# Performance work log

Hardware: AMD Instinct MI355X
Metric: run time of the kernel (lower is better)

## Reference

```python
import jax, jax.numpy as jnp
import numpy as np

B, T, D, H = 8, 4096, 512, 512


def setup_inputs() -> dict:
    key = jax.random.key(0)
    k1, k2, k3, k4, k5, k6 = jax.random.split(key, 6)
    lim = 1.0 / np.sqrt(D)
    return {
        "x": jax.random.normal(k1, (B, T, D), dtype=jnp.float32),
        "h_0": jax.random.normal(k2, (B, 1, H), dtype=jnp.float32),
        "W_z": jax.random.uniform(k3, (H, D), jnp.float32, -lim, lim),
        "b_z": jax.random.uniform(k4, (H,), jnp.float32, -lim, lim),
        "W_h": jax.random.uniform(k5, (H, D), jnp.float32, -lim, lim),
        "b_h": jax.random.uniform(k6, (H,), jnp.float32, -lim, lim),
    }


def reference(x, h_0, W_z, b_z, W_h, b_h):
    # z_t = sigmoid(W_z x_t), h~_t = tanh(W_h x_t)
    z = jax.nn.sigmoid(jnp.einsum('btd,hd->bth', x, W_z) + b_z)  # (B,T,H)
    h_tilde = jnp.tanh(jnp.einsum('btd,hd->bth', x, W_h) + b_h)  # (B,T,H)
    a = 1.0 - z            # multiplicative coeffs
    b = z * h_tilde        # additive terms (b[:,0] handled as h0 carry)

    # linear recurrence h_t = a_t * h_{t-1} + b_t, h_0 given
    def scan_fn(h_prev, ab):
        a_t, b_t = ab
        h_t = a_t * h_prev + b_t
        return h_t, h_t

    a_t = jnp.swapaxes(a, 0, 1)  # (T,B,H)
    b_t = jnp.swapaxes(b, 0, 1)  # (T,B,H)
    _, hs = jax.lax.scan(scan_fn, h_0[:, 0, :], (a_t, b_t))
    return jnp.swapaxes(hs, 0, 1)  # (B,T,H)
```

## Files before the change

### kernel.cpp

```cpp
#include <hip/hip_runtime.h>

constexpr int Bn = 8, Tn = 4096, Dn = 512, Hn = 512;
constexpr int Mn = Bn * Tn;
constexpr int BM = 128, BHt = 128, BK = 32;
constexpr int NKT = Dn / BK;
constexpr int CH = 64, NC = Tn / CH;

typedef __attribute__((ext_vector_type(8))) short s8v;
typedef __attribute__((ext_vector_type(4))) float f4v;
typedef __attribute__((ext_vector_type(8))) _Float16 h8v;
typedef unsigned short ushort_t;

__device__ __forceinline__ short f2bf(float f) {
  unsigned u = __float_as_uint(f);
  u = (u + 0x7fffu + ((u >> 16) & 1u)) >> 16;
  return (short)u;
}

__global__ __launch_bounds__(256) void convert_all(
    const float* __restrict__ X, const float* __restrict__ Wz,
    const float* __restrict__ Wh, ushort_t* __restrict__ Xb,
    ushort_t* __restrict__ Wzb, ushort_t* __restrict__ Whb) {
  int bx = blockIdx.x, tid = threadIdx.x;
  const float* src;
  ushort_t* dst;
  int lb;
  if (bx < 4096)      { src = X;  dst = Xb;  lb = bx; }
  else if (bx < 4160) { src = Wz; dst = Wzb; lb = bx - 4096; }
  else                { src = Wh; dst = Whb; lb = bx - 4160; }
  const float* tsrc = src + ((size_t)(lb >> 4) * 128) * Dn + (lb & 15) * BK;
#pragma unroll
  for (int p = 0; p < 2; p++) {
    int idx = tid + p * 256;
    int r = idx >> 2, k8 = idx & 3;
    const float4* sv = reinterpret_cast<const float4*>(tsrc + (size_t)r * Dn + k8 * 8);
    float4 f0 = sv[0], f1 = sv[1];
    s8v v;
    v[0] = f2bf(f0.x); v[1] = f2bf(f0.y); v[2] = f2bf(f0.z); v[3] = f2bf(f0.w);
    v[4] = f2bf(f1.x); v[5] = f2bf(f1.y); v[6] = f2bf(f1.z); v[7] = f2bf(f1.w);
    int c = (r >> 4) * 64 + k8 * 16 + (r & 15);
    *reinterpret_cast<s8v*>(&dst[((size_t)lb * 512 + c) * 8]) = v;
  }
}

__global__ __launch_bounds__(256, 2) void gemm_act(
    const ushort_t* __restrict__ Xb, const ushort_t* __restrict__ Wzb,
    const ushort_t* __restrict__ Whb,
    const float* __restrict__ bzp, const float* __restrict__ bhp,
    h8v* __restrict__ cab) {
  int tid = threadIdx.x, lane = tid & 63, wid = tid >> 6;
  int wr = wid >> 1, wc = wid & 1;
  int bm = blockIdx.x, bhb = blockIdx.y;

  const s8v* xs = reinterpret_cast<const s8v*>(Xb) + (size_t)bm * NKT * 512 + (wr * 4) * 64 + lane;
  const s8v* zs = reinterpret_cast<const s8v*>(Wzb) + (size_t)bhb * NKT * 512 + (wc * 4) * 64 + lane;
  const s8v* hs = reinterpret_cast<const s8v*>(Whb) + (size_t)bhb * NKT * 512 + (wc * 4) * 64 + lane;

  f4v accz[4][4], acch[4][4];
#pragma unroll
  for (int i = 0; i < 4; i++)
#pragma unroll
    for (int j = 0; j < 4; j++) {
      accz[i][j] = (f4v){0.f, 0.f, 0.f, 0.f};
      acch[i][j] = (f4v){0.f, 0.f, 0.f, 0.f};
    }

#pragma unroll 2
  for (int ks = 0; ks < NKT; ks++) {
    s8v af[4], bzf[4], bhf[4];
#pragma unroll
    for (int i = 0; i < 4; i++) af[i] = xs[ks * 512 + i * 64];
#pragma unroll
    for (int j = 0; j < 4; j++) {
      bzf[j] = zs[ks * 512 + j * 64];
      bhf[j] = hs[ks * 512 + j * 64];
    }
#pragma unroll
    for (int i = 0; i < 4; i++)
#pragma unroll
      for (int j = 0; j < 4; j++) {
        accz[i][j] = __builtin_amdgcn_mfma_f32_16x16x32_bf16(af[i], bzf[j], accz[i][j], 0, 0, 0);
        acch[i][j] = __builtin_amdgcn_mfma_f32_16x16x32_bf16(af[i], bhf[j], acch[i][j], 0, 0, 0);
      }
  }

  int R = bm * 2 + wr, Cc = bhb * 2 + wc;
  size_t base = (size_t)(R * 8 + Cc) * 1024;
  float bzv[4], bhv[4];
#pragma unroll
  for (int j = 0; j < 4; j++) {
    int h = bhb * BHt + wc * 64 + j * 16 + (lane & 15);
    bzv[j] = bzp[h];
    bhv[j] = bhp[h];
  }
#pragma unroll
  for (int i = 0; i < 4; i++)
#pragma unroll
    for (int j = 0; j < 4; j++) {
      h8v g;
#pragma unroll
      for (int q = 0; q < 4; q++) {
        float z = 1.f / (1.f + __expf(-(accz[i][j][q] + bzv[j])));
        float e = __expf(2.f * (acch[i][j][q] + bhv[j]));
        float th = 1.f - 2.f / (e + 1.f);
        g[q] = (_Float16)(1.f - z);
        g[4 + q] = (_Float16)(z * th);
      }
      cab[base + (size_t)((i * 4 + j) * 64 + lane)] = g;
    }
}

__global__ __launch_bounds__(256) void scan_chunk(
    const h8v* __restrict__ cab, float* __restrict__ cA, float* __restrict__ cB) {
  int h = blockIdx.y * 256 + threadIdx.x;
  int R = blockIdx.x;
  int hl = h & 63, Cc = h >> 6;
  size_t base = (size_t)(R * 8 + Cc) * 1024 + (size_t)(hl >> 4) * 64 + (hl & 15);
  float A = 1.f, Bv = 0.f;
#pragma unroll
  for (int i = 0; i < 4; i++)
#pragma unroll
    for (int p = 0; p < 4; p++) {
      h8v g = cab[base + i * 256 + p * 16];
#pragma unroll
      for (int q = 0; q < 4; q++) {
        float a = (float)g[q], b = (float)g[4 + q];
        A *= a;
        Bv = fmaf(a, Bv, b);
      }
    }
  cA[(size_t)R * Hn + h] = A;
  cB[(size_t)R * Hn + h] = Bv;
}

__global__ __launch_bounds__(256) void scan_heads(
    const float* __restrict__ cA, const float* __restrict__ cB,
    const float* __restrict__ h0p, float* __restrict__ hst) {
  int gid = blockIdx.x * 256 + threadIdx.x;
  int b = gid >> 9, h = gid & 511;
  float hr = h0p[(size_t)b * Hn + h];
#pragma unroll 8
  for (int c = 0; c < NC; c++) {
    size_t o = (size_t)(b * NC + c) * Hn + h;
    hst[o] = hr;
    hr = fmaf(cA[o], hr, cB[o]);
  }
}

__global__ __launch_bounds__(256) void scan_apply(
    const h8v* __restrict__ cab, const float* __restrict__ hst,
    float* __restrict__ out) {
  int h = blockIdx.y * 256 + threadIdx.x;
  int R = blockIdx.x;
  int hl = h & 63, Cc = h >> 6;
  size_t base = (size_t)(R * 8 + Cc) * 1024 + (size_t)(hl >> 4) * 64 + (hl & 15);
  float hr = hst[(size_t)R * Hn + h];
  size_t ob = (size_t)R * 64 * Hn + h;
#pragma unroll
  for (int i = 0; i < 4; i++)
#pragma unroll
    for (int p = 0; p < 4; p++) {
      h8v g = cab[base + i * 256 + p * 16];
#pragma unroll
      for (int q = 0; q < 4; q++) {
        hr = fmaf((float)g[q], hr, (float)g[4 + q]);
        out[ob + (size_t)(i * 16 + p * 4 + q) * Hn] = hr;
      }
    }
}

extern "C" void kernel_launch(void* const* d_in, const int* in_sizes, int n_in,
                              void* d_out, int out_size, void* d_ws, size_t ws_size,
                              hipStream_t stream) {
  const float* X   = (const float*)d_in[0];
  const float* h0p = (const float*)d_in[1];
  const float* Wz  = (const float*)d_in[2];
  const float* bz  = (const float*)d_in[3];
  const float* Wh  = (const float*)d_in[4];
  const float* bh  = (const float*)d_in[5];
  float* out = (float*)d_out;

  char* ws = (char*)d_ws;
  ushort_t* Xb  = (ushort_t*)ws;
  ushort_t* Wzb = Xb + (size_t)Mn * Dn;
  ushort_t* Whb = Wzb + (size_t)Hn * Dn;
  h8v* cab      = (h8v*)(Whb + (size_t)Hn * Dn);
  float* cA     = (float*)(cab + (size_t)Mn * Hn / 4);
  float* cB     = cA + (size_t)Bn * NC * Hn;
  float* hst    = cB + (size_t)Bn * NC * Hn;

  convert_all<<<dim3(4224), 256, 0, stream>>>(X, Wz, Wh, Xb, Wzb, Whb);

  gemm_act<<<dim3(Mn / BM, Hn / BHt), 256, 0, stream>>>(Xb, Wzb, Whb, bz, bh, cab);

  scan_chunk<<<dim3(Mn / 64, Hn / 256), 256, 0, stream>>>(cab, cA, cB);
  scan_heads<<<dim3(Bn * Hn / 256), 256, 0, stream>>>(cA, cB, h0p, hst);
  scan_apply<<<dim3(Mn / 64, Hn / 256), 256, 0, stream>>>(cab, hst, out);
}
```

Before: 105.7 us.

## Fuse chunk scan into GEMM epilogue and software-pipeline fragment loads

Computes per-chunk scan aggregates (product of a, combined b) directly in the GEMM epilogue using in-register composition and cross-lane shuffles, removing the separate scan_chunk kernel and its re-read of the cab buffer. The K loop is also restructured into a double-buffered prefetch of the next k-step's fragments, interleaved with the MFMA groups so global loads overlap compute. This costs extra registers in an already register-heavy kernel, which may lower occupancy.

```diff
diff --git a/kernel.cpp b/kernel.cpp
--- a/kernel.cpp
+++ b/kernel.cpp
@@ -47,7 +47,7 @@
     const ushort_t* __restrict__ Xb, const ushort_t* __restrict__ Wzb,
     const ushort_t* __restrict__ Whb,
     const float* __restrict__ bzp, const float* __restrict__ bhp,
-    h8v* __restrict__ cab) {
+    h8v* __restrict__ cab, float* __restrict__ cA, float* __restrict__ cB) {
   int tid = threadIdx.x, lane = tid & 63, wid = tid >> 6;
   int wr = wid >> 1, wc = wid & 1;
   int bm = blockIdx.x, bhb = blockIdx.y;
@@ -65,23 +65,52 @@
       acch[i][j] = (f4v){0.f, 0.f, 0.f, 0.f};
     }
 
-#pragma unroll 2
-  for (int ks = 0; ks < NKT; ks++) {
-    s8v af[4], bzf[4], bhf[4];
-#pragma unroll
-    for (int i = 0; i < 4; i++) af[i] = xs[ks * 512 + i * 64];
-#pragma unroll
-    for (int j = 0; j < 4; j++) {
-      bzf[j] = zs[ks * 512 + j * 64];
-      bhf[j] = hs[ks * 512 + j * 64];
-    }
-#pragma unroll
-    for (int i = 0; i < 4; i++)
-#pragma unroll
-      for (int j = 0; j < 4; j++) {
-        accz[i][j] = __builtin_amdgcn_mfma_f32_16x16x32_bf16(af[i], bzf[j], accz[i][j], 0, 0, 0);
-        acch[i][j] = __builtin_amdgcn_mfma_f32_16x16x32_bf16(af[i], bhf[j], acch[i][j], 0, 0, 0);
-      }
+  s8v afA[4], bzA[4], afB[4], bzB[4], bhf[4];
+#pragma unroll
+  for (int i = 0; i < 4; i++) afA[i] = xs[i * 64];
+#pragma unroll
+  for (int j = 0; j < 4; j++) bzA[j] = zs[j * 64];
+#pragma unroll
+  for (int j = 0; j < 4; j++) bhf[j] = hs[j * 64];
+
+#pragma unroll
+  for (int ks = 0; ks < NKT; ks += 2) {
+#pragma unroll
+    for (int i = 0; i < 4; i++) afB[i] = xs[(ks + 1) * 512 + i * 64];
+#pragma unroll
+    for (int j = 0; j < 4; j++) bzB[j] = zs[(ks + 1) * 512 + j * 64];
+#pragma unroll
+    for (int i = 0; i < 4; i++)
+#pragma unroll
+      for (int j = 0; j < 4; j++)
+        accz[i][j] = __builtin_amdgcn_mfma_f32_16x16x32_bf16(afA[i], bzA[j], accz[i][j], 0, 0, 0);
+#pragma unroll
+    for (int i = 0; i < 4; i++)
+#pragma unroll
+      for (int j = 0; j < 4; j++)
+        acch[i][j] = __builtin_amdgcn_mfma_f32_16x16x32_bf16(afA[i], bhf[j], acch[i][j], 0, 0, 0);
+#pragma unroll
+    for (int j = 0; j < 4; j++) bhf[j] = hs[(ks + 1) * 512 + j * 64];
+    if (ks + 2 < NKT) {
+#pragma unroll
+      for (int i = 0; i < 4; i++) afA[i] = xs[(ks + 2) * 512 + i * 64];
+#pragma unroll
+      for (int j = 0; j < 4; j++) bzA[j] = zs[(ks + 2) * 512 + j * 64];
+    }
+#pragma unroll
+    for (int i = 0; i < 4; i++)
+#pragma unroll
+      for (int j = 0; j < 4; j++)
+        accz[i][j] = __builtin_amdgcn_mfma_f32_16x16x32_bf16(afB[i], bzB[j], accz[i][j], 0, 0, 0);
+#pragma unroll
+    for (int i = 0; i < 4; i++)
+#pragma unroll
+      for (int j = 0; j < 4; j++)
+        acch[i][j] = __builtin_amdgcn_mfma_f32_16x16x32_bf16(afB[i], bhf[j], acch[i][j], 0, 0, 0);
+    if (ks + 2 < NKT) {
+#pragma unroll
+      for (int j = 0; j < 4; j++) bhf[j] = hs[(ks + 2) * 512 + j * 64];
+    }
   }
 
   int R = bm * 2 + wr, Cc = bhb * 2 + wc;
@@ -93,11 +122,13 @@
     bzv[j] = bzp[h];
     bhv[j] = bhp[h];
   }
+  float QA[4][4], QB[4][4];
 #pragma unroll
   for (int i = 0; i < 4; i++)
 #pragma unroll
     for (int j = 0; j < 4; j++) {
       h8v g;
+      float Pa = 1.f, Pb = 0.f;
 #pragma unroll
       for (int q = 0; q < 4; q++) {
         float z = 1.f / (1.f + __expf(-(accz[i][j][q] + bzv[j])));
@@ -105,32 +136,40 @@
         float th = 1.f - 2.f / (e + 1.f);
         g[q] = (_Float16)(1.f - z);
         g[4 + q] = (_Float16)(z * th);
+        float a = (float)g[q], b = (float)g[4 + q];
+        Pa = a * Pa;
+        Pb = a * Pb + b;
       }
       cab[base + (size_t)((i * 4 + j) * 64 + lane)] = g;
-    }
-}
-
-__global__ __launch_bounds__(256) void scan_chunk(
-    const h8v* __restrict__ cab, float* __restrict__ cA, float* __restrict__ cB) {
-  int h = blockIdx.y * 256 + threadIdx.x;
-  int R = blockIdx.x;
-  int hl = h & 63, Cc = h >> 6;
-  size_t base = (size_t)(R * 8 + Cc) * 1024 + (size_t)(hl >> 4) * 64 + (hl & 15);
-  float A = 1.f, Bv = 0.f;
-#pragma unroll
-  for (int i = 0; i < 4; i++)
-#pragma unroll
-    for (int p = 0; p < 4; p++) {
-      h8v g = cab[base + i * 256 + p * 16];
-#pragma unroll
-      for (int q = 0; q < 4; q++) {
-        float a = (float)g[q], b = (float)g[4 + q];
-        A *= a;
-        Bv = fmaf(a, Bv, b);
-      }
-    }
-  cA[(size_t)R * Hn + h] = A;
-  cB[(size_t)R * Hn + h] = Bv;
+      QA[i][j] = Pa;
+      QB[i][j] = Pb;
+    }
+
+#pragma unroll
+  for (int j = 0; j < 4; j++) {
+    float A = 1.f, Bv = 0.f;
+#pragma unroll
+    for (int i = 0; i < 4; i++) {
+      float a = QA[i][j], b = QB[i][j];
+      float ap = __shfl_xor(a, 16), bp = __shfl_xor(b, 16);
+      bool hi = (lane & 16) != 0;
+      float af_ = hi ? ap : a, bf_ = hi ? bp : b;
+      float as_ = hi ? a : ap, bs_ = hi ? b : bp;
+      a = as_ * af_; b = as_ * bf_ + bs_;
+      ap = __shfl_xor(a, 32); bp = __shfl_xor(b, 32);
+      bool hi2 = (lane & 32) != 0;
+      af_ = hi2 ? ap : a; bf_ = hi2 ? bp : b;
+      as_ = hi2 ? a : ap; bs_ = hi2 ? b : bp;
+      a = as_ * af_; b = as_ * bf_ + bs_;
+      Bv = a * Bv + b;
+      A = a * A;
+    }
+    if (lane < 16) {
+      int h = bhb * BHt + wc * 64 + j * 16 + lane;
+      cA[(size_t)R * Hn + h] = A;
+      cB[(size_t)R * Hn + h] = Bv;
+    }
+  }
 }
 
 __global__ __launch_bounds__(256) void scan_heads(
@@ -191,9 +230,8 @@
 
   convert_all<<<dim3(4224), 256, 0, stream>>>(X, Wz, Wh, Xb, Wzb, Whb);
 
-  gemm_act<<<dim3(Mn / BM, Hn / BHt), 256, 0, stream>>>(Xb, Wzb, Whb, bz, bh, cab);
-
-  scan_chunk<<<dim3(Mn / 64, Hn / 256), 256, 0, stream>>>(cab, cA, cB);
+  gemm_act<<<dim3(Mn / BM, Hn / BHt), 256, 0, stream>>>(Xb, Wzb, Whb, bz, bh, cab, cA, cB);
+
   scan_heads<<<dim3(Bn * Hn / 256), 256, 0, stream>>>(cA, cB, h0p, hst);
   scan_apply<<<dim3(Mn / 64, Hn / 256), 256, 0, stream>>>(cab, hst, out);
 }
```

After: 99.33 us. 1.06x faster.
